# Kernel optimization log

Hardware: AMD Instinct MI355X
Metric: run time of the kernel (lower is better)

The kernel has to match this reference:

```python
import jax, jax.numpy as jnp
import numpy as np

B, C, HW, A, E, H1, HID = 4096, 4, 64, 32, 4, 1024, 512


def setup_inputs() -> dict:
    key = jax.random.key(0)
    ks = jax.random.split(key, 16)
    def rn(k, shape, fan_in):
        return jax.random.normal(k, shape, dtype=jnp.float32) / np.sqrt(fan_in)
    inp = {
        "x": jax.random.normal(ks[0], (B, C, HW, HW), dtype=jnp.float32),
        # conv stack (OIHW)
        "cW1": rn(ks[1], (32, C, 8, 8), C * 64), "cb1": 0.1 * jnp.ones((32,), jnp.float32),
        "cW2": rn(ks[2], (64, 32, 4, 4), 32 * 16), "cb2": 0.1 * jnp.ones((64,), jnp.float32),
        "cW3": rn(ks[3], (64, 64, 3, 3), 64 * 9), "cb3": 0.1 * jnp.ones((64,), jnp.float32),
        # E expert advantage streams: Linear(1024->512), relu, Linear(512->A)
        "aW1": rn(ks[4], (E, H1, HID), H1), "ab1": jnp.zeros((E, HID), jnp.float32),
        "aW2": rn(ks[5], (E, HID, A), HID), "ab2": jnp.zeros((E, A), jnp.float32),
        # E expert value streams: Linear(1024->512), relu, Linear(512->1)
        "vW1": rn(ks[6], (E, H1, HID), H1), "vb1": jnp.zeros((E, HID), jnp.float32),
        "vW2": rn(ks[7], (E, HID, 1), HID), "vb2": jnp.zeros((E, 1), jnp.float32),
        # reward bucket boundaries (buffer): boundaries * scale - 1e-8
        "boundaries": jnp.array([-0.5, 0.0, 0.5], jnp.float32) * 1.0 - 1e-8,
    }
    return inp


def _conv(h, W, b, stride):
    out = jax.lax.conv_general_dilated(h, W, (stride, stride), "VALID",
                                       dimension_numbers=("NCHW", "OIHW", "NCHW"))
    return out + b[None, :, None, None]


def _routed_mlp(h, W1, b1, W2, b2, idx):
    # h: [B, H1]; W1: [E, H1, HID]; W2: [E, HID, O]; idx: [B]
    # Compute all experts (E is tiny), then gather the routed output per sample.
    z = jax.nn.relu(jnp.einsum("bi,eio->ebo", h, W1) + b1[:, None, :])  # [E,B,HID]
    y = jnp.einsum("ebo,eoa->eba", z, W2) + b2[:, None, :]              # [E,B,O]
    return y[idx, jnp.arange(h.shape[0])]                                # [B,O]


def reference(x, cW1, cb1, cW2, cb2, cW3, cb3, aW1, ab1, aW2, ab2,
              vW1, vb1, vW2, vb2, boundaries):
    h = jax.nn.relu(_conv(x, cW1, cb1, 4))   # [B,32,15,15]
    h = jax.nn.relu(_conv(h, cW2, cb2, 2))   # [B,64,6,6]
    h = jax.nn.relu(_conv(h, cW3, cb3, 1))   # [B,64,4,4]
    bsz = x.shape[0]
    h = h.reshape(bsz, -1)                   # [B,1024]
    rewards = x[:, -1, 0, 0]                 # [B]
    idx = jnp.sum(rewards[:, None] > boundaries[None, :], axis=1)  # [B] in [0,E)
    ya = _routed_mlp(h, aW1, ab1, aW2, ab2, idx)  # [B,A]
    mean = jnp.sum(ya, axis=1, keepdims=True) / ya.shape[1]
    ys = _routed_mlp(h, vW1, vb1, vW2, vb2, idx)  # [B,1]
    q = (ya - mean) + ys
    return q
```

## Files before the change

kernel.cpp:

```cpp
#include <hip/hip_runtime.h>
#include <hip/hip_bf16.h>

typedef __bf16 bf16;
typedef bf16 bf16x8 __attribute__((ext_vector_type(8)));
typedef bf16 bf16x4 __attribute__((ext_vector_type(4)));
typedef float f32x4 __attribute__((ext_vector_type(4)));

__device__ __forceinline__ int SZ(int a) { return a ^ (((a >> 7) & 7) << 4); }

__global__ __launch_bounds__(256) void k_pre(const float* __restrict__ cW1,
    const float* __restrict__ cW2, const float* __restrict__ cW3,
    bf16* __restrict__ W1p, bf16* __restrict__ W2p, bf16* __restrict__ W3p) {
  const int bid = blockIdx.x, tid = threadIdx.x;
  if (bid < 32) {
    int i = bid * 256 + tid;
    int oc = i >> 8, k = i & 255;
    int ic = k & 3, kp = k >> 2, kx = kp & 7, ky = kp >> 3;
    W1p[i] = (bf16)cW1[oc * 256 + ic * 64 + ky * 8 + kx];
  } else if (bid < 160) {
    int i = (bid - 32) * 256 + tid;
    int oc = i >> 9, k = i & 511;
    int ic = k & 31, kp = k >> 5, kx = kp & 3, ky = kp >> 2;
    W2p[i] = (bf16)cW2[oc * 512 + ic * 16 + ky * 4 + kx];
  } else {
    int i = (bid - 160) * 256 + tid;
    if (i < 36864) {
      int oc = i / 576, k = i - oc * 576;
      int ic = k & 63, kp = k >> 6, kx = kp % 3, ky = kp / 3;
      W3p[i] = (bf16)cW3[oc * 576 + ic * 9 + ky * 3 + kx];
    }
  }
}

__global__ __launch_bounds__(256) void k_pre2(const float* __restrict__ aW1,
    const float* __restrict__ vW1, bf16* __restrict__ W1T) {
  __shared__ float t[64][65];
  const int bid2 = blockIdx.x;
  const int bz = bid2 >> 7, rest = bid2 & 127, by = rest >> 4, bx = rest & 15;
  const float* in = (bz >= 4 ? vW1 : aW1) + (size_t)(bz & 3) * 524288;
  const int k0 = bx * 64, n0 = by * 64;
  const int tid = threadIdx.x, cc = tid & 63, r0 = (tid >> 6) * 16;
  for (int i = 0; i < 16; ++i)
    t[r0 + i][cc] = in[(size_t)(k0 + r0 + i) * 512 + n0 + cc];
  __syncthreads();
  for (int i = 0; i < 16; ++i) {
    int n = r0 + i, k = cc;
    W1T[((size_t)bz * 512 + n0 + n) * 1024 + k0 + k] = (bf16)t[k][n];
  }
}

__global__ __launch_bounds__(256) void k_route_cls(const float* __restrict__ x,
    const float* __restrict__ bd, int* __restrict__ ecls) {
  const int b = blockIdx.x * 256 + threadIdx.x;
  const float r = x[(size_t)b * 16384 + 12288];
  ecls[b] = (r > bd[0]) + (r > bd[1]) + (r > bd[2]);
}

__global__ __launch_bounds__(1024) void k_route_scan(const int* __restrict__ ecls,
    int* __restrict__ perm, int* __restrict__ cnt) {
  const int tid = threadIdx.x;
  const int4 ev = ((const int4*)ecls)[tid];
  int e[4] = {ev.x, ev.y, ev.z, ev.w};
  int lc[4] = {0, 0, 0, 0};
  #pragma unroll
  for (int i = 0; i < 4; ++i) lc[e[i]]++;
  const int lane = tid & 63, wv = tid >> 6;
  __shared__ int wsum[16][4];
  __shared__ int wbase[16][4];
  int pre[4];
  #pragma unroll
  for (int q = 0; q < 4; ++q) {
    int v = lc[q];
    #pragma unroll
    for (int d = 1; d < 64; d <<= 1) {
      int u = __shfl_up(v, d);
      if (lane >= d) v += u;
    }
    pre[q] = v - lc[q];
    if (lane == 63) wsum[wv][q] = v;
  }
  __syncthreads();
  if (tid == 0) {
    int tot[4] = {0, 0, 0, 0};
    for (int w = 0; w < 16; ++w)
      #pragma unroll
      for (int q = 0; q < 4; ++q) { wbase[w][q] = tot[q]; tot[q] += wsum[w][q]; }
    #pragma unroll
    for (int q = 0; q < 4; ++q) cnt[q] = tot[q];
  }
  __syncthreads();
  int run[4];
  #pragma unroll
  for (int q = 0; q < 4; ++q) run[q] = wbase[wv][q] + pre[q];
  #pragma unroll
  for (int i = 0; i < 4; ++i) {
    const int b = tid * 4 + i;
    perm[e[i] * 4096 + run[e[i]]] = b;
    run[e[i]]++;
  }
}

__global__ __launch_bounds__(256, 3) void k_conv123(const float* __restrict__ x,
    const bf16* __restrict__ W1p, const float* __restrict__ b1,
    const bf16* __restrict__ W2p, const float* __restrict__ b2,
    const bf16* __restrict__ W3p, const float* __restrict__ b3,
    bf16* __restrict__ h3) {
  __shared__ bf16 sA[16384];
  __shared__ bf16 sh1[9000];
  const int b = blockIdx.x, tid = threadIdx.x;
  const int lane = tid & 63, wave = tid >> 6, lid = lane & 15, c = lane >> 4;

  {
    bf16x8 bw[8];
    const int ot = wave & 1, col = ot * 16 + lid;
    #pragma unroll
    for (int ks = 0; ks < 8; ++ks) bw[ks] = *(const bf16x8*)(W1p + col * 256 + ks * 32 + c * 8);
    const float bias = b1[col];
    #pragma unroll
    for (int ks = 0; ks < 8; ++ks) asm volatile("" : "+v"(bw[ks]));

    const float4* xs = (const float4*)(x + (size_t)b * 16384);
    #pragma unroll
    for (int hb = 0; hb < 2; ++hb) {
      float4 r[2][4];
      #pragma unroll
      for (int h = 0; h < 2; ++h)
        #pragma unroll
        for (int ic = 0; ic < 4; ++ic)
          r[h][ic] = xs[ic * 1024 + tid + (hb * 2 + h) * 256];
      #pragma unroll
      for (int h = 0; h < 2; ++h) {
        const int g = tid + (hb * 2 + h) * 256;
        bf16x8 lo, hi;
        lo[0] = (bf16)r[h][0].x; lo[1] = (bf16)r[h][1].x; lo[2] = (bf16)r[h][2].x; lo[3] = (bf16)r[h][3].x;
        lo[4] = (bf16)r[h][0].y; lo[5] = (bf16)r[h][1].y; lo[6] = (bf16)r[h][2].y; lo[7] = (bf16)r[h][3].y;
        hi[0] = (bf16)r[h][0].z; hi[1] = (bf16)r[h][1].z; hi[2] = (bf16)r[h][2].z; hi[3] = (bf16)r[h][3].z;
        hi[4] = (bf16)r[h][0].w; hi[5] = (bf16)r[h][1].w; hi[6] = (bf16)r[h][2].w; hi[7] = (bf16)r[h][3].w;
        *(bf16x8*)((char*)sA + SZ(g * 32))      = lo;
        *(bf16x8*)((char*)sA + SZ(g * 32 + 16)) = hi;
      }
    }
    __syncthreads();

    int ab[8], ptv[8];
    #pragma unroll
    for (int pi = 0; pi < 8; ++pi) {
      int pt = (wave >> 1) + 2 * pi; if (pt > 14) pt = 14;
      ptv[pi] = pt;
      int p = pt * 16 + lid; if (p > 224) p = 224;
      const int py = p / 15, px = p - py * 15;
      ab[pi] = py * 2048 + px * 32 + c * 16;
    }
    f32x4 acc[8];
    #pragma unroll
    for (int pi = 0; pi < 8; ++pi) acc[pi] = (f32x4){0.f, 0.f, 0.f, 0.f};
    #pragma unroll
    for (int ks = 0; ks < 8; ++ks)
      #pragma unroll
      for (int pi = 0; pi < 8; ++pi)
        acc[pi] = __builtin_amdgcn_mfma_f32_16x16x32_bf16(
            *(const bf16x8*)((const char*)sA + SZ(ab[pi] + ks * 512)), bw[ks], acc[pi], 0, 0, 0);
    __syncthreads();
    #pragma unroll
    for (int pi = 0; pi < 8; ++pi)
      #pragma unroll
      for (int r = 0; r < 4; ++r) {
        const int pr = ptv[pi] * 16 + c * 4 + r;
        if (pr < 225) sh1[pr * 40 + col] = (bf16)fmaxf(acc[pi][r] + bias, 0.f);
      }
  }
  __syncthreads();

  bf16* sh2 = sA;
  const int col = wave * 16 + lid;
  {
    bf16x8 bw2[16];
    #pragma unroll
    for (int ks = 0; ks < 16; ++ks) bw2[ks] = *(const bf16x8*)(W2p + col * 512 + ks * 32 + c * 8);
    const float bias2 = b2[col];
    #pragma unroll
    for (int ks = 0; ks < 16; ++ks) asm volatile("" : "+v"(bw2[ks]));

    int abase[3];
    #pragma unroll
    for (int pt = 0; pt < 3; ++pt) {
      int p = pt * 16 + lid; if (p > 35) p = 35;
      const int oy = p / 6, ox = p - oy * 6;
      abase[pt] = (oy * 30 + ox * 2) * 40 + c * 8;
    }
    f32x4 acc2[3];
    #pragma unroll
    for (int pt = 0; pt < 3; ++pt) acc2[pt] = (f32x4){0.f, 0.f, 0.f, 0.f};
    #pragma unroll
    for (int ks = 0; ks < 16; ++ks) {
      const int ky = ks >> 2, kx = ks & 3;
      #pragma unroll
      for (int pt = 0; pt < 3; ++pt)
        acc2[pt] = __builtin_amdgcn_mfma_f32_16x16x32_bf16(
            *(const bf16x8*)(&sh1[abase[pt] + (ky * 15 + kx) * 40]), bw2[ks], acc2[pt], 0, 0, 0);
    }
    #pragma unroll
    for (int pt = 0; pt < 3; ++pt)
      #pragma unroll
      for (int r = 0; r < 4; ++r) {
        const int pr = pt * 16 + c * 4 + r;
        if (pr < 36) sh2[pr * 72 + col] = (bf16)fmaxf(acc2[pt][r] + bias2, 0.f);
      }
  }
  __syncthreads();

  {
    bf16x8 bw3[18];
    #pragma unroll
    for (int ks = 0; ks < 18; ++ks) bw3[ks] = *(const bf16x8*)(W3p + col * 576 + ks * 32 + c * 8);
    const float bias3 = b3[col];
    #pragma unroll
    for (int ks = 0; ks < 18; ++ks) asm volatile("" : "+v"(bw3[ks]));
    const int oy = lid >> 2, ox = lid & 3;
    const int ab3 = (oy * 6 + ox) * 72 + c * 8;
    f32x4 acc = {0.f, 0.f, 0.f, 0.f};
    #pragma unroll
    for (int ks = 0; ks < 18; ++ks) {
      const int kp = ks >> 1, ky = kp / 3, kx = kp - ky * 3;
      acc = __builtin_amdgcn_mfma_f32_16x16x32_bf16(
          *(const bf16x8*)(&sh2[ab3 + (ky * 6 + kx) * 72 + (ks & 1) * 32]), bw3[ks], acc, 0, 0, 0);
    }
    bf16x4 o;
    #pragma unroll
    for (int r = 0; r < 4; ++r) o[r] = (bf16)fmaxf(acc[r] + bias3, 0.f);
    *(bf16x4*)(h3 + (size_t)b * 1024 + col * 16 + c * 4) = o;
  }
}

__global__ __launch_bounds__(512) void k_mlp1(const bf16* __restrict__ h3,
    const bf16* __restrict__ W1T, const float* __restrict__ ab1, const float* __restrict__ vb1,
    const int* __restrict__ perm, const int* __restrict__ cnt,
    bf16* __restrict__ za, bf16* __restrict__ zv) {
  const int e = blockIdx.z;
  const int cntE = cnt[e];
  const int m0 = blockIdx.x * 64;
  if (m0 >= cntE) return;
  const int n0 = blockIdx.y * 128;
  const bf16* WA = W1T + (size_t)e * 524288;
  const bf16* WV = W1T + (size_t)(4 + e) * 524288;

  __shared__ bf16 As[64 * 72];
  __shared__ int rows[64];
  const int tid = threadIdx.x;
  if (tid < 64) {
    int j = m0 + tid; if (j > cntE - 1) j = cntE - 1;
    rows[tid] = perm[e * 4096 + j];
  }
  __syncthreads();

  const int lane = tid & 63, wave = tid >> 6;
  const int lid = lane & 15, c = lane >> 4;
  const int wm = wave >> 2, wn = wave & 3;
  const int srow = tid >> 3, skoff = (tid & 7) * 8;
  const bf16* arow = h3 + (size_t)rows[srow] * 1024 + skoff;
  const int colA = n0 + wn * 32 + lid;
  const bf16* wa0 = WA + (size_t)colA * 1024 + c * 8;
  const bf16* wa1 = WA + (size_t)(colA + 16) * 1024 + c * 8;
  const bf16* wv0 = WV + (size_t)colA * 1024 + c * 8;
  const bf16* wv1 = WV + (size_t)(colA + 16) * 1024 + c * 8;
  const int ar0 = (wm * 32 + lid) * 72 + c * 8;
  const int ar1 = (wm * 32 + 16 + lid) * 72 + c * 8;

  f32x4 acc[2][2][2];
  #pragma unroll
  for (int n = 0; n < 2; ++n)
    #pragma unroll
    for (int m = 0; m < 2; ++m)
      #pragma unroll
      for (int f = 0; f < 2; ++f) acc[n][m][f] = (f32x4){0.f, 0.f, 0.f, 0.f};

  for (int k0 = 0; k0 < 1024; k0 += 64) {
    *(bf16x8*)(&As[srow * 72 + skoff]) = *(const bf16x8*)(arow + k0);
    __syncthreads();
    bf16x8 a[2][2];
    #pragma unroll
    for (int m = 0; m < 2; ++m)
      #pragma unroll
      for (int ks = 0; ks < 2; ++ks)
        a[m][ks] = *(const bf16x8*)(&As[(m ? ar1 : ar0) + ks * 32]);
    #pragma unroll
    for (int ks = 0; ks < 2; ++ks) {
      bf16x8 bA0 = *(const bf16x8*)(wa0 + k0 + ks * 32);
      bf16x8 bA1 = *(const bf16x8*)(wa1 + k0 + ks * 32);
      bf16x8 bV0 = *(const bf16x8*)(wv0 + k0 + ks * 32);
      bf16x8 bV1 = *(const bf16x8*)(wv1 + k0 + ks * 32);
      #pragma unroll
      for (int m = 0; m < 2; ++m) {
        acc[0][m][0] = __builtin_amdgcn_mfma_f32_16x16x32_bf16(a[m][ks], bA0, acc[0][m][0], 0, 0, 0);
        acc[0][m][1] = __builtin_amdgcn_mfma_f32_16x16x32_bf16(a[m][ks], bA1, acc[0][m][1], 0, 0, 0);
        acc[1][m][0] = __builtin_amdgcn_mfma_f32_16x16x32_bf16(a[m][ks], bV0, acc[1][m][0], 0, 0, 0);
        acc[1][m][1] = __builtin_amdgcn_mfma_f32_16x16x32_bf16(a[m][ks], bV1, acc[1][m][1], 0, 0, 0);
      }
    }
    __syncthreads();
  }

  #pragma unroll
  for (int cf = 0; cf < 2; ++cf) {
    const int col = colA + cf * 16;
    const float bA = ab1[e * 512 + col];
    const float bV = vb1[e * 512 + col];
    #pragma unroll
    for (int m = 0; m < 2; ++m)
      #pragma unroll
      for (int r = 0; r < 4; ++r) {
        const int ridx = wm * 32 + m * 16 + c * 4 + r;
        if (m0 + ridx < cntE) {
          const size_t zoff = (size_t)rows[ridx] * 512 + col;
          za[zoff] = (bf16)fmaxf(acc[0][m][cf][r] + bA, 0.f);
          zv[zoff] = (bf16)fmaxf(acc[1][m][cf][r] + bV, 0.f);
        }
      }
  }
}

__global__ __launch_bounds__(256) void k_mlp2(const bf16* __restrict__ za,
    const bf16* __restrict__ zv,
    const float* __restrict__ aW2, const float* __restrict__ ab2,
    const float* __restrict__ vW2, const float* __restrict__ vb2,
    const int* __restrict__ perm, const int* __restrict__ cnt,
    float* __restrict__ out) {
  const int e = blockIdx.y;
  const int cntE = cnt[e];
  const int m0 = blockIdx.x * 64;
  if (m0 >= cntE) return;
  __shared__ bf16 Bs[48 * 520];
  const int tid = threadIdx.x;
  for (int i = tid; i < 512 * 32; i += 256) {
    const int k = i >> 5, n = i & 31;
    Bs[n * 520 + k] = (bf16)aW2[(size_t)e * 16384 + i];
  }
  for (int i = tid; i < 512; i += 256) Bs[32 * 520 + i] = (bf16)vW2[e * 512 + i];
  for (int i = tid; i < 15 * 512; i += 256) {
    const int n = 33 + (i >> 9), k = i & 511;
    Bs[n * 520 + k] = (bf16)0.f;
  }
  __syncthreads();

  const int lane = tid & 63, wave = tid >> 6;
  const int lid = lane & 15, c = lane >> 4;
  const int row0 = m0 + wave * 16;
  if (row0 >= cntE) return;
  int rowl = row0 + lid; if (rowl > cntE - 1) rowl = cntE - 1;
  const int pb = perm[e * 4096 + rowl];
  const bf16* aA = za + (size_t)pb * 512 + c * 8;
  const bf16* aV = zv + (size_t)pb * 512 + c * 8;

  f32x4 acc0 = {0.f, 0.f, 0.f, 0.f}, acc1 = acc0, accv = acc0;
  #pragma unroll
  for (int k0 = 0; k0 < 512; k0 += 32) {
    bf16x8 a1 = *(const bf16x8*)(aA + k0);
    bf16x8 a2 = *(const bf16x8*)(aV + k0);
    bf16x8 b0 = *(const bf16x8*)(&Bs[lid * 520 + k0 + c * 8]);
    bf16x8 b1 = *(const bf16x8*)(&Bs[(16 + lid) * 520 + k0 + c * 8]);
    bf16x8 b2 = *(const bf16x8*)(&Bs[(32 + lid) * 520 + k0 + c * 8]);
    acc0 = __builtin_amdgcn_mfma_f32_16x16x32_bf16(a1, b0, acc0, 0, 0, 0);
    acc1 = __builtin_amdgcn_mfma_f32_16x16x32_bf16(a1, b1, acc1, 0, 0, 0);
    accv = __builtin_amdgcn_mfma_f32_16x16x32_bf16(a2, b2, accv, 0, 0, 0);
  }

  const float ba0 = ab2[e * 32 + lid], ba1 = ab2[e * 32 + 16 + lid], bv = vb2[e];
  #pragma unroll
  for (int r = 0; r < 4; ++r) {
    const int row = row0 + c * 4 + r;
    const float y0 = acc0[r] + ba0, y1 = acc1[r] + ba1;
    float s = y0 + y1;
    s += __shfl_xor(s, 1); s += __shfl_xor(s, 2);
    s += __shfl_xor(s, 4); s += __shfl_xor(s, 8);
    const float mean = s * 0.03125f;
    const float ys = __shfl(accv[r], lane & 48) + bv;
    if (row < cntE) {
      const int bq = perm[e * 4096 + row];
      out[(size_t)bq * 32 + lid] = y0 - mean + ys;
      out[(size_t)bq * 32 + 16 + lid] = y1 - mean + ys;
    }
  }
}

extern "C" void kernel_launch(void* const* d_in, const int* in_sizes, int n_in,
                              void* d_out, int out_size, void* d_ws, size_t ws_size,
                              hipStream_t stream) {
  const float* x   = (const float*)d_in[0];
  const float* cW1 = (const float*)d_in[1];
  const float* cb1 = (const float*)d_in[2];
  const float* cW2 = (const float*)d_in[3];
  const float* cb2 = (const float*)d_in[4];
  const float* cW3 = (const float*)d_in[5];
  const float* cb3 = (const float*)d_in[6];
  const float* aW1 = (const float*)d_in[7];
  const float* ab1 = (const float*)d_in[8];
  const float* aW2 = (const float*)d_in[9];
  const float* ab2 = (const float*)d_in[10];
  const float* vW1 = (const float*)d_in[11];
  const float* vb1 = (const float*)d_in[12];
  const float* vW2 = (const float*)d_in[13];
  const float* vb2 = (const float*)d_in[14];
  const float* bd  = (const float*)d_in[15];
  float* out = (float*)d_out;

  char* ws = (char*)d_ws;
  bf16* W1T = (bf16*)(ws);
  bf16* za  = (bf16*)(ws + 8388608ull);
  bf16* zv  = (bf16*)(ws + 12582912ull);
  bf16* h3  = (bf16*)(ws + 16777216ull);
  bf16* W1p = (bf16*)(ws + 25165824ull);
  bf16* W2p = (bf16*)(ws + 25182208ull);
  bf16* W3p = (bf16*)(ws + 25247744ull);
  int* perm = (int*)(ws + 25321472ull);
  int* cnt  = (int*)(ws + 25387008ull);
  int* ecls = (int*)(ws + 25387072ull);

  k_route_cls<<<16, 256, 0, stream>>>(x, bd, ecls);
  k_pre<<<304, 256, 0, stream>>>(cW1, cW2, cW3, W1p, W2p, W3p);
  k_pre2<<<1024, 256, 0, stream>>>(aW1, vW1, W1T);
  k_route_scan<<<1, 1024, 0, stream>>>(ecls, perm, cnt);
  k_conv123<<<4096, 256, 0, stream>>>(x, W1p, cb1, W2p, cb2, W3p, cb3, h3);
  k_mlp1<<<dim3(64, 4, 4), 512, 0, stream>>>(h3, W1T, ab1, vb1, perm, cnt, za, zv);
  k_mlp2<<<dim3(64, 4), 256, 0, stream>>>(za, zv, aW2, ab2, vW2, vb2, perm, cnt, out);
}
```

Before: 206.6 us.

## Split conv1 input staging into two halves to overlap loads with MFMA

The conv1 stage now loads and stages only the rows needed for the first half of output rows into one LDS buffer, computes them, then converts and stores the prefetched second half into a separate buffer. The global loads for the second half are issued before the first-half MFMAs, so their latency is hidden behind compute. Conv1 is also reorganized so each wave computes full output rows for both 16-channel tiles, sharing the A fragment between the two tiles. __syncthreads is replaced by an explicit lgkmcnt wait plus s_barrier. This costs more registers for the prefetched data and two weight sets, which may reduce occupancy under the launch bound of 3 blocks.

```diff
diff --git a/kernel.cpp b/kernel.cpp
--- a/kernel.cpp
+++ b/kernel.cpp
@@ -105,73 +105,125 @@
     const bf16* __restrict__ W2p, const float* __restrict__ b2,
     const bf16* __restrict__ W3p, const float* __restrict__ b3,
     bf16* __restrict__ h3) {
-  __shared__ bf16 sA[16384];
+  __shared__ bf16 sA0[9216];
+  __shared__ bf16 sA1[8192];
   __shared__ bf16 sh1[9000];
   const int b = blockIdx.x, tid = threadIdx.x;
   const int lane = tid & 63, wave = tid >> 6, lid = lane & 15, c = lane >> 4;
+  const float4* xs = (const float4*)(x + (size_t)b * 16384);
 
   {
-    bf16x8 bw[8];
-    const int ot = wave & 1, col = ot * 16 + lid;
-    #pragma unroll
-    for (int ks = 0; ks < 8; ++ks) bw[ks] = *(const bf16x8*)(W1p + col * 256 + ks * 32 + c * 8);
-    const float bias = b1[col];
-    #pragma unroll
-    for (int ks = 0; ks < 8; ++ks) asm volatile("" : "+v"(bw[ks]));
-
-    const float4* xs = (const float4*)(x + (size_t)b * 16384);
-    #pragma unroll
-    for (int hb = 0; hb < 2; ++hb) {
-      float4 r[2][4];
-      #pragma unroll
-      for (int h = 0; h < 2; ++h)
+    float4 rv[3][4];
+    #pragma unroll
+    for (int i = 0; i < 3; ++i) {
+      const int g = tid + i * 256;
+      if (g < 576)
         #pragma unroll
-        for (int ic = 0; ic < 4; ++ic)
-          r[h][ic] = xs[ic * 1024 + tid + (hb * 2 + h) * 256];
-      #pragma unroll
-      for (int h = 0; h < 2; ++h) {
-        const int g = tid + (hb * 2 + h) * 256;
+        for (int ic = 0; ic < 4; ++ic) rv[i][ic] = xs[ic * 1024 + g];
+    }
+    #pragma unroll
+    for (int i = 0; i < 3; ++i) {
+      const int g = tid + i * 256;
+      if (g < 576) {
         bf16x8 lo, hi;
-        lo[0] = (bf16)r[h][0].x; lo[1] = (bf16)r[h][1].x; lo[2] = (bf16)r[h][2].x; lo[3] = (bf16)r[h][3].x;
-        lo[4] = (bf16)r[h][0].y; lo[5] = (bf16)r[h][1].y; lo[6] = (bf16)r[h][2].y; lo[7] = (bf16)r[h][3].y;
-        hi[0] = (bf16)r[h][0].z; hi[1] = (bf16)r[h][1].z; hi[2] = (bf16)r[h][2].z; hi[3] = (bf16)r[h][3].z;
-        hi[4] = (bf16)r[h][0].w; hi[5] = (bf16)r[h][1].w; hi[6] = (bf16)r[h][2].w; hi[7] = (bf16)r[h][3].w;
-        *(bf16x8*)((char*)sA + SZ(g * 32))      = lo;
-        *(bf16x8*)((char*)sA + SZ(g * 32 + 16)) = hi;
-      }
-    }
-    __syncthreads();
-
-    int ab[8], ptv[8];
-    #pragma unroll
-    for (int pi = 0; pi < 8; ++pi) {
-      int pt = (wave >> 1) + 2 * pi; if (pt > 14) pt = 14;
-      ptv[pi] = pt;
-      int p = pt * 16 + lid; if (p > 224) p = 224;
-      const int py = p / 15, px = p - py * 15;
-      ab[pi] = py * 2048 + px * 32 + c * 16;
-    }
-    f32x4 acc[8];
-    #pragma unroll
-    for (int pi = 0; pi < 8; ++pi) acc[pi] = (f32x4){0.f, 0.f, 0.f, 0.f};
-    #pragma unroll
-    for (int ks = 0; ks < 8; ++ks)
-      #pragma unroll
-      for (int pi = 0; pi < 8; ++pi)
-        acc[pi] = __builtin_amdgcn_mfma_f32_16x16x32_bf16(
-            *(const bf16x8*)((const char*)sA + SZ(ab[pi] + ks * 512)), bw[ks], acc[pi], 0, 0, 0);
-    __syncthreads();
-    #pragma unroll
-    for (int pi = 0; pi < 8; ++pi)
+        lo[0] = (bf16)rv[i][0].x; lo[1] = (bf16)rv[i][1].x; lo[2] = (bf16)rv[i][2].x; lo[3] = (bf16)rv[i][3].x;
+        lo[4] = (bf16)rv[i][0].y; lo[5] = (bf16)rv[i][1].y; lo[6] = (bf16)rv[i][2].y; lo[7] = (bf16)rv[i][3].y;
+        hi[0] = (bf16)rv[i][0].z; hi[1] = (bf16)rv[i][1].z; hi[2] = (bf16)rv[i][2].z; hi[3] = (bf16)rv[i][3].z;
+        hi[4] = (bf16)rv[i][0].w; hi[5] = (bf16)rv[i][1].w; hi[6] = (bf16)rv[i][2].w; hi[7] = (bf16)rv[i][3].w;
+        *(bf16x8*)((char*)sA0 + SZ(g * 32))      = lo;
+        *(bf16x8*)((char*)sA0 + SZ(g * 32 + 16)) = hi;
+      }
+    }
+  }
+
+  float4 r1v[2][4];
+  #pragma unroll
+  for (int i = 0; i < 2; ++i) {
+    const int g = tid + i * 256;
+    #pragma unroll
+    for (int ic = 0; ic < 4; ++ic) r1v[i][ic] = xs[ic * 1024 + 512 + g];
+  }
+
+  bf16x8 bw[2][8];
+  float bias01[2];
+  #pragma unroll
+  for (int ot = 0; ot < 2; ++ot) {
+    const int col = ot * 16 + lid;
+    #pragma unroll
+    for (int ky = 0; ky < 8; ++ky)
+      bw[ot][ky] = *(const bf16x8*)(W1p + col * 256 + ky * 32 + c * 8);
+    bias01[ot] = b1[col];
+  }
+
+  asm volatile("s_waitcnt lgkmcnt(0)" ::: "memory");
+  __builtin_amdgcn_s_barrier();
+
+  const int colc = (lid < 14) ? lid : 14;
+  {
+    #pragma unroll
+    for (int rr = 0; rr < 2; ++rr) {
+      const int row = wave * 2 + rr;
+      f32x4 a0 = {0.f, 0.f, 0.f, 0.f}, a1 = {0.f, 0.f, 0.f, 0.f};
+      #pragma unroll
+      for (int ky = 0; ky < 8; ++ky) {
+        bf16x8 av = *(const bf16x8*)((const char*)sA0 + SZ((row * 4 + ky) * 512 + colc * 32 + c * 16));
+        a0 = __builtin_amdgcn_mfma_f32_16x16x32_bf16(av, bw[0][ky], a0, 0, 0, 0);
+        a1 = __builtin_amdgcn_mfma_f32_16x16x32_bf16(av, bw[1][ky], a1, 0, 0, 0);
+      }
       #pragma unroll
       for (int r = 0; r < 4; ++r) {
-        const int pr = ptv[pi] * 16 + c * 4 + r;
-        if (pr < 225) sh1[pr * 40 + col] = (bf16)fmaxf(acc[pi][r] + bias, 0.f);
-      }
-  }
-  __syncthreads();
-
-  bf16* sh2 = sA;
+        const int pc = c * 4 + r;
+        if (pc < 15) {
+          const int p = row * 15 + pc;
+          sh1[p * 40 + lid]      = (bf16)fmaxf(a0[r] + bias01[0], 0.f);
+          sh1[p * 40 + 16 + lid] = (bf16)fmaxf(a1[r] + bias01[1], 0.f);
+        }
+      }
+    }
+  }
+
+  #pragma unroll
+  for (int i = 0; i < 2; ++i) {
+    const int g = tid + i * 256;
+    bf16x8 lo, hi;
+    lo[0] = (bf16)r1v[i][0].x; lo[1] = (bf16)r1v[i][1].x; lo[2] = (bf16)r1v[i][2].x; lo[3] = (bf16)r1v[i][3].x;
+    lo[4] = (bf16)r1v[i][0].y; lo[5] = (bf16)r1v[i][1].y; lo[6] = (bf16)r1v[i][2].y; lo[7] = (bf16)r1v[i][3].y;
+    hi[0] = (bf16)r1v[i][0].z; hi[1] = (bf16)r1v[i][1].z; hi[2] = (bf16)r1v[i][2].z; hi[3] = (bf16)r1v[i][3].z;
+    hi[4] = (bf16)r1v[i][0].w; hi[5] = (bf16)r1v[i][1].w; hi[6] = (bf16)r1v[i][2].w; hi[7] = (bf16)r1v[i][3].w;
+    *(bf16x8*)((char*)sA1 + SZ(g * 32))      = lo;
+    *(bf16x8*)((char*)sA1 + SZ(g * 32 + 16)) = hi;
+  }
+
+  asm volatile("s_waitcnt lgkmcnt(0)" ::: "memory");
+  __builtin_amdgcn_s_barrier();
+
+  {
+    #pragma unroll
+    for (int rr = 0; rr < 2; ++rr) {
+      int row = 8 + wave * 2 + rr; if (row > 14) row = 14;
+      f32x4 a0 = {0.f, 0.f, 0.f, 0.f}, a1 = {0.f, 0.f, 0.f, 0.f};
+      #pragma unroll
+      for (int ky = 0; ky < 8; ++ky) {
+        bf16x8 av = *(const bf16x8*)((const char*)sA1 + SZ((row * 4 + ky - 32) * 512 + colc * 32 + c * 16));
+        a0 = __builtin_amdgcn_mfma_f32_16x16x32_bf16(av, bw[0][ky], a0, 0, 0, 0);
+        a1 = __builtin_amdgcn_mfma_f32_16x16x32_bf16(av, bw[1][ky], a1, 0, 0, 0);
+      }
+      #pragma unroll
+      for (int r = 0; r < 4; ++r) {
+        const int pc = c * 4 + r;
+        if (pc < 15) {
+          const int p = row * 15 + pc;
+          sh1[p * 40 + lid]      = (bf16)fmaxf(a0[r] + bias01[0], 0.f);
+          sh1[p * 40 + 16 + lid] = (bf16)fmaxf(a1[r] + bias01[1], 0.f);
+        }
+      }
+    }
+  }
+
+  asm volatile("s_waitcnt lgkmcnt(0)" ::: "memory");
+  __builtin_amdgcn_s_barrier();
+
+  bf16* sh2 = sA0;
   const int col = wave * 16 + lid;
   {
     bf16x8 bw2[16];
@@ -207,7 +259,9 @@
         if (pr < 36) sh2[pr * 72 + col] = (bf16)fmaxf(acc2[pt][r] + bias2, 0.f);
       }
   }
-  __syncthreads();
+
+  asm volatile("s_waitcnt lgkmcnt(0)" ::: "memory");
+  __builtin_amdgcn_s_barrier();
 
   {
     bf16x8 bw3[18];
```

Result: slower. 219.9 us (+6.4%).

## Merge routing classification and W1 transpose into the conv kernel launch

Applied to the files above, without the earlier changes.

Folds the route classification kernel and the expert W1 transpose/bf16 conversion kernel into the conv kernel as extra leading blocks, dispatching on block index. This removes two kernel launches and lets these small, independent jobs overlap with the conv work instead of running serially. The route scan now runs after conv finishes, which delays nothing since mlp1 needs h3 anyway. The transpose blocks reuse the conv shared buffer and are bound by the conv kernel's launch bounds and register allocation.

```diff
diff --git a/kernel.cpp b/kernel.cpp
--- a/kernel.cpp
+++ b/kernel.cpp
@@ -32,30 +32,6 @@
   }
 }
 
-__global__ __launch_bounds__(256) void k_pre2(const float* __restrict__ aW1,
-    const float* __restrict__ vW1, bf16* __restrict__ W1T) {
-  __shared__ float t[64][65];
-  const int bid2 = blockIdx.x;
-  const int bz = bid2 >> 7, rest = bid2 & 127, by = rest >> 4, bx = rest & 15;
-  const float* in = (bz >= 4 ? vW1 : aW1) + (size_t)(bz & 3) * 524288;
-  const int k0 = bx * 64, n0 = by * 64;
-  const int tid = threadIdx.x, cc = tid & 63, r0 = (tid >> 6) * 16;
-  for (int i = 0; i < 16; ++i)
-    t[r0 + i][cc] = in[(size_t)(k0 + r0 + i) * 512 + n0 + cc];
-  __syncthreads();
-  for (int i = 0; i < 16; ++i) {
-    int n = r0 + i, k = cc;
-    W1T[((size_t)bz * 512 + n0 + n) * 1024 + k0 + k] = (bf16)t[k][n];
-  }
-}
-
-__global__ __launch_bounds__(256) void k_route_cls(const float* __restrict__ x,
-    const float* __restrict__ bd, int* __restrict__ ecls) {
-  const int b = blockIdx.x * 256 + threadIdx.x;
-  const float r = x[(size_t)b * 16384 + 12288];
-  ecls[b] = (r > bd[0]) + (r > bd[1]) + (r > bd[2]);
-}
-
 __global__ __launch_bounds__(1024) void k_route_scan(const int* __restrict__ ecls,
     int* __restrict__ perm, int* __restrict__ cnt) {
   const int tid = threadIdx.x;
@@ -100,14 +76,41 @@
   }
 }
 
-__global__ __launch_bounds__(256, 3) void k_conv123(const float* __restrict__ x,
+__global__ __launch_bounds__(256, 3) void k_front(const float* __restrict__ x,
+    const float* __restrict__ bd, int* __restrict__ ecls,
+    const float* __restrict__ aW1, const float* __restrict__ vW1, bf16* __restrict__ W1T,
     const bf16* __restrict__ W1p, const float* __restrict__ b1,
     const bf16* __restrict__ W2p, const float* __restrict__ b2,
     const bf16* __restrict__ W3p, const float* __restrict__ b3,
     bf16* __restrict__ h3) {
   __shared__ bf16 sA[16384];
   __shared__ bf16 sh1[9000];
-  const int b = blockIdx.x, tid = threadIdx.x;
+  const int bid = blockIdx.x, tid = threadIdx.x;
+
+  if (bid < 16) {
+    const int b = bid * 256 + tid;
+    const float r = x[(size_t)b * 16384 + 12288];
+    ecls[b] = (r > bd[0]) + (r > bd[1]) + (r > bd[2]);
+    return;
+  }
+  if (bid < 1040) {
+    float* t = (float*)sA;
+    const int bid2 = bid - 16;
+    const int bz = bid2 >> 7, rest = bid2 & 127, by = rest >> 4, bx = rest & 15;
+    const float* in = (bz >= 4 ? vW1 : aW1) + (size_t)(bz & 3) * 524288;
+    const int k0 = bx * 64, n0 = by * 64;
+    const int cc = tid & 63, r0 = (tid >> 6) * 16;
+    for (int i = 0; i < 16; ++i)
+      t[(r0 + i) * 65 + cc] = in[(size_t)(k0 + r0 + i) * 512 + n0 + cc];
+    __syncthreads();
+    for (int i = 0; i < 16; ++i) {
+      int n = r0 + i, k = cc;
+      W1T[((size_t)bz * 512 + n0 + n) * 1024 + k0 + k] = (bf16)t[k * 65 + n];
+    }
+    return;
+  }
+
+  const int b = bid - 1040;
   const int lane = tid & 63, wave = tid >> 6, lid = lane & 15, c = lane >> 4;
 
   {
@@ -415,11 +418,10 @@
   int* cnt  = (int*)(ws + 25387008ull);
   int* ecls = (int*)(ws + 25387072ull);
 
-  k_route_cls<<<16, 256, 0, stream>>>(x, bd, ecls);
   k_pre<<<304, 256, 0, stream>>>(cW1, cW2, cW3, W1p, W2p, W3p);
-  k_pre2<<<1024, 256, 0, stream>>>(aW1, vW1, W1T);
+  k_front<<<5136, 256, 0, stream>>>(x, bd, ecls, aW1, vW1, W1T,
+                                    W1p, cb1, W2p, cb2, W3p, cb3, h3);
   k_route_scan<<<1, 1024, 0, stream>>>(ecls, perm, cnt);
-  k_conv123<<<4096, 256, 0, stream>>>(x, W1p, cb1, W2p, cb2, W3p, cb3, h3);
   k_mlp1<<<dim3(64, 4, 4), 512, 0, stream>>>(h3, W1T, ab1, vb1, perm, cnt, za, zv);
   k_mlp2<<<dim3(64, 4), 256, 0, stream>>>(za, zv, aW2, ab2, vW2, vb2, perm, cnt, out);
 }
```

Measured after the change: 200.2 us, median of 2. 3.1% less time.
